# Kernel optimization log

Measured on AMD Instinct MI355X. Metric: run time of the kernel, lower is better.

Reference implementation:

```python
import jax, jax.numpy as jnp
import numpy as np

EPS = 1e-5

def _lc(x, w, b, stride, pad):
    # x: [B,H,W]; w: [Ho,Wo,kh,kw]; b: [Ho,Wo]
    Ho, Wo, kh, kw = w.shape
    patches = jax.lax.conv_general_dilated_patches(
        x[:, None], (kh, kw), (stride, stride), [(pad, pad), (pad, pad)])
    # patches: [B, kh*kw, Ho, Wo]
    out = jnp.einsum('bkij,ijk->bij', patches, w.reshape(Ho, Wo, kh * kw))
    return out + b

def _ln2d(x, g, b):
    # torch LayerNorm over the last two (spatial) dims
    mu = x.mean(axis=(1, 2), keepdims=True)
    var = ((x - mu) ** 2).mean(axis=(1, 2), keepdims=True)
    return (x - mu) * jax.lax.rsqrt(var + EPS) * g + b

def _pool(x):
    # MaxPool2d(kernel=2, stride=2) over spatial dims of [B,H,W]
    return jax.lax.reduce_window(x, -jnp.inf, jax.lax.max, (1, 2, 2), (1, 2, 2), 'VALID')

def setup_inputs() -> dict:
    key = jax.random.key(0)
    ks = jax.random.split(key, 32)
    d = {}
    d['x'] = jax.random.normal(ks[0], (64, 128, 128), jnp.float32)
    sizes = [(128, 7), (64, 5), (64, 5), (32, 3), (32, 3), (16, 3)]
    for i, (s, k) in enumerate(sizes, start=1):
        d[f'w{i}'] = jax.random.normal(ks[4 * i], (s, s, k, k), jnp.float32) / k
        d[f'b{i}'] = jax.random.normal(ks[4 * i + 1], (s, s), jnp.float32)
        d[f'g{i}'] = jnp.ones((s, s), jnp.float32)
        d[f'be{i}'] = jnp.zeros((s, s), jnp.float32)
    d['fcw'] = jax.random.normal(ks[30], (1024, 256), jnp.float32) / np.sqrt(256.0)
    d['fcb'] = jax.random.normal(ks[31], (1024,), jnp.float32) * 0.01
    return d

def reference(x, w1, b1, g1, be1, w2, b2, g2, be2, w3, b3, g3, be3,
              w4, b4, g4, be4, w5, b5, g5, be5, w6, b6, g6, be6, fcw, fcb):
    # dropout is identity (eval / p=0)
    h = _pool(_ln2d(jax.nn.relu(_lc(x, w1, b1, 1, 3)), g1, be1))   # [B,64,64]
    h = _ln2d(jax.nn.relu(_lc(h, w2, b2, 1, 2)), g2, be2)          # [B,64,64]
    h = _pool(_ln2d(jax.nn.relu(_lc(h, w3, b3, 1, 2)), g3, be3))   # [B,32,32]
    h = _ln2d(jax.nn.relu(_lc(h, w4, b4, 1, 1)), g4, be4)          # [B,32,32]
    h = _pool(_ln2d(jax.nn.relu(_lc(h, w5, b5, 1, 1)), g5, be5))   # [B,16,16]
    h = _ln2d(jax.nn.relu(_lc(h, w6, b6, 1, 1)), g6, be6)          # [B,16,16]
    h = h.reshape(h.shape[0], -1) @ fcw.T + fcb                    # [B,1024]
    return jax.nn.softmax(h, axis=-1)
```

## Files before the change

kernel.cpp:

```cpp
#include <hip/hip_runtime.h>

#define LN_EPS 1e-5f

template<int RIN, bool POOL, bool FIRST, int K, int TILE, int S>
__launch_bounds__(256)
__global__ void lc_stage(const float* __restrict__ in,
                         const float* __restrict__ pstats,
                         const float* __restrict__ gamma,
                         const float* __restrict__ beta,
                         const float* __restrict__ w,
                         const float* __restrict__ bias,
                         float* __restrict__ out,
                         float* __restrict__ stats)
{
    constexpr int CIN  = POOL ? RIN / 2 : RIN;
    constexpr int ROUT = CIN;
    constexpr int PAD  = (K - 1) / 2;
    constexpr int RT   = TILE + K - 1;
    constexpr int PP   = RT * RT + 1;
    constexpr int NBLK = ROUT / TILE;
    constexpr int WCNT = TILE * TILE * K * K;
    constexpr int SG   = 64 / S;
    constexpr int PG   = 256 / S;
    constexpr int OPT  = (TILE * TILE >= PG) ? (TILE * TILE) / PG : 1;
    constexpr float INV_NPREV = 1.0f / (float)(RIN * RIN);

    struct WB { float w[WCNT]; float b[TILE * TILE]; };
    union UU { WB wb; float red[512]; };

    __shared__ float s_in[S * PP];
    __shared__ UU    s_u;
    __shared__ float s_mean[S], s_rstd[S];

    const int tid = threadIdx.x;
    const int bt  = blockIdx.x % (NBLK * NBLK);
    const int sg  = blockIdx.x / (NBLK * NBLK);
    const int i0  = (bt / NBLK) * TILE;
    const int j0  = (bt % NBLK) * TILE;
    const int S0  = sg * S;

    if constexpr (!FIRST) {
        if (tid < S) {
            float mu  = pstats[S0 + tid] * INV_NPREV;
            float msq = pstats[64 + S0 + tid] * INV_NPREV;
            s_mean[tid] = mu;
            s_rstd[tid] = 1.0f / sqrtf(msq - mu * mu + LN_EPS);
        }
        __syncthreads();
    }

    for (int idx = tid; idx < WCNT; idx += 256) {
        int pi = idx / (K * K);
        int kk = idx % (K * K);
        int gi = i0 + pi / TILE, gj = j0 + pi % TILE;
        s_u.wb.w[idx] = w[(gi * ROUT + gj) * (K * K) + kk];
    }
    if (tid < TILE * TILE) {
        int gi = i0 + tid / TILE, gj = j0 + tid % TILE;
        s_u.wb.b[tid] = bias[gi * ROUT + gj];
    }

    for (int idx = tid; idx < S * RT * RT; idx += 256) {
        int ls = idx / (RT * RT);
        int p  = idx % (RT * RT);
        int rr = p / RT, rc = p % RT;
        int ci = i0 - PAD + rr, cj = j0 - PAD + rc;
        float val = 0.0f;
        if (ci >= 0 && ci < CIN && cj >= 0 && cj < CIN) {
            if constexpr (FIRST) {
                val = in[(S0 + ls) * RIN * RIN + ci * RIN + cj];
            } else if constexpr (POOL) {
                float mu = s_mean[ls], rs = s_rstd[ls];
                float best = -3.4e38f;
                #pragma unroll
                for (int dy = 0; dy < 2; dy++) {
                    #pragma unroll
                    for (int dx = 0; dx < 2; dx++) {
                        int ry = 2 * ci + dy, rx = 2 * cj + dx;
                        float raw = in[(S0 + ls) * RIN * RIN + ry * RIN + rx];
                        float n = (raw - mu) * rs * gamma[ry * RIN + rx] + beta[ry * RIN + rx];
                        best = fmaxf(best, n);
                    }
                }
                val = best;
            } else {
                float mu = s_mean[ls], rs = s_rstd[ls];
                float raw = in[(S0 + ls) * RIN * RIN + ci * RIN + cj];
                val = (raw - mu) * rs * gamma[ci * RIN + cj] + beta[ci * RIN + cj];
            }
        }
        s_in[ls * PP + p] = val;
    }
    __syncthreads();

    const int s  = tid % S;
    const int pg = tid / S;
    const int p0 = pg * OPT;
    float lsum = 0.0f, lsq = 0.0f;
    if (p0 < TILE * TILE) {
        const int ti  = p0 / TILE;
        const int tj0 = p0 % TILE;
        float acc[OPT];
        #pragma unroll
        for (int o = 0; o < OPT; o++) acc[o] = s_u.wb.b[p0 + o];
        #pragma unroll
        for (int ki = 0; ki < K; ki++) {
            float row[OPT + K - 1];
            #pragma unroll
            for (int c = 0; c < OPT + K - 1; c++)
                row[c] = s_in[s * PP + (ti + ki) * RT + tj0 + c];
            #pragma unroll
            for (int kj = 0; kj < K; kj++)
                #pragma unroll
                for (int o = 0; o < OPT; o++)
                    acc[o] += row[o + kj] * s_u.wb.w[(p0 + o) * (K * K) + ki * K + kj];
        }
        #pragma unroll
        for (int o = 0; o < OPT; o++) {
            float v = fmaxf(acc[o], 0.0f);
            out[(S0 + s) * ROUT * ROUT + (i0 + ti) * ROUT + (j0 + tj0 + o)] = v;
            lsum += v;
            lsq  += v * v;
        }
    }

    __syncthreads();
    s_u.red[tid]       = lsum;
    s_u.red[256 + tid] = lsq;
    __syncthreads();
    if (tid < S) {
        float a = 0.0f, b = 0.0f;
        #pragma unroll
        for (int g = 0; g < PG; g++) {
            a += s_u.red[g * S + tid];
            b += s_u.red[256 + g * S + tid];
        }
        atomicAdd(&stats[S0 + tid], a);
        atomicAdd(&stats[64 + S0 + tid], b);
    }
}

__launch_bounds__(256)
__global__ void fc_logits(const float* __restrict__ t6,
                          const float* __restrict__ stats6,
                          const float* __restrict__ g6,
                          const float* __restrict__ be6,
                          const float* __restrict__ fcw,
                          const float* __restrict__ fcb,
                          float* __restrict__ logits)
{
    __shared__ float h[256];
    const int s   = blockIdx.x >> 2;
    const int q   = blockIdx.x & 3;
    const int tid = threadIdx.x;

    float mu  = stats6[s] * (1.0f / 256.0f);
    float msq = stats6[64 + s] * (1.0f / 256.0f);
    float rstd = 1.0f / sqrtf(msq - mu * mu + LN_EPS);
    h[tid] = (t6[s * 256 + tid] - mu) * rstd * g6[tid] + be6[tid];
    __syncthreads();

    const int o = q * 256 + tid;
    const float4* wr = (const float4*)(fcw + o * 256);
    float acc = 0.0f;
    #pragma unroll 8
    for (int k = 0; k < 64; k++) {
        float4 wv = wr[k];
        acc += wv.x * h[4 * k] + wv.y * h[4 * k + 1] + wv.z * h[4 * k + 2] + wv.w * h[4 * k + 3];
    }
    logits[s * 1024 + o] = acc + fcb[o];
}

__launch_bounds__(256)
__global__ void softmax_k(const float* __restrict__ logits,
                          float* __restrict__ out)
{
    __shared__ float red[256];
    const int s   = blockIdx.x;
    const int tid = threadIdx.x;

    float4 v = ((const float4*)(logits + s * 1024))[tid];
    float lmax = fmaxf(fmaxf(v.x, v.y), fmaxf(v.z, v.w));
    red[tid] = lmax;
    __syncthreads();
    for (int off = 128; off > 0; off >>= 1) {
        if (tid < off) red[tid] = fmaxf(red[tid], red[tid + off]);
        __syncthreads();
    }
    float M = red[0];
    __syncthreads();

    float4 e;
    e.x = expf(v.x - M); e.y = expf(v.y - M);
    e.z = expf(v.z - M); e.w = expf(v.w - M);
    red[tid] = e.x + e.y + e.z + e.w;
    __syncthreads();
    for (int off = 128; off > 0; off >>= 1) {
        if (tid < off) red[tid] += red[tid + off];
        __syncthreads();
    }
    float inv = 1.0f / red[0];
    e.x *= inv; e.y *= inv; e.z *= inv; e.w *= inv;
    ((float4*)(out + s * 1024))[tid] = e;
}

extern "C" void kernel_launch(void* const* d_in, const int* in_sizes, int n_in,
                              void* d_out, int out_size, void* d_ws, size_t ws_size,
                              hipStream_t stream) {
    (void)in_sizes; (void)n_in; (void)out_size; (void)ws_size;

    const float* x   = (const float*)d_in[0];
    const float* w1  = (const float*)d_in[1];
    const float* b1  = (const float*)d_in[2];
    const float* g1  = (const float*)d_in[3];
    const float* be1 = (const float*)d_in[4];
    const float* w2  = (const float*)d_in[5];
    const float* b2  = (const float*)d_in[6];
    const float* g2  = (const float*)d_in[7];
    const float* be2 = (const float*)d_in[8];
    const float* w3  = (const float*)d_in[9];
    const float* b3  = (const float*)d_in[10];
    const float* g3  = (const float*)d_in[11];
    const float* be3 = (const float*)d_in[12];
    const float* w4  = (const float*)d_in[13];
    const float* b4  = (const float*)d_in[14];
    const float* g4  = (const float*)d_in[15];
    const float* be4 = (const float*)d_in[16];
    const float* w5  = (const float*)d_in[17];
    const float* b5  = (const float*)d_in[18];
    const float* g5  = (const float*)d_in[19];
    const float* be5 = (const float*)d_in[20];
    const float* w6  = (const float*)d_in[21];
    const float* b6  = (const float*)d_in[22];
    const float* g6  = (const float*)d_in[23];
    const float* be6 = (const float*)d_in[24];
    const float* fcw = (const float*)d_in[25];
    const float* fcb = (const float*)d_in[26];

    float* ws = (float*)d_ws;
    float* t1 = ws;
    float* t2 = t1 + 64 * 128 * 128;
    float* t3 = t2 + 64 * 64 * 64;
    float* t4 = t3 + 64 * 64 * 64;
    float* t5 = t4 + 64 * 32 * 32;
    float* t6 = t5 + 64 * 32 * 32;
    float* st = t6 + 64 * 16 * 16;

    hipMemsetAsync(st, 0, 6 * 128 * sizeof(float), stream);

    lc_stage<128, false, true,  7, 8, 16><<<1024, 256, 0, stream>>>(x,  nullptr,  nullptr, nullptr, w1, b1, t1, st + 0);
    lc_stage<128, true,  false, 5, 4, 16><<<1024, 256, 0, stream>>>(t1, st + 0,   g1, be1, w2, b2, t2, st + 128);
    lc_stage<64,  false, false, 5, 4, 16><<<1024, 256, 0, stream>>>(t2, st + 128, g2, be2, w3, b3, t3, st + 256);
    lc_stage<64,  true,  false, 3, 4, 16><<<256,  256, 0, stream>>>(t3, st + 256, g3, be3, w4, b4, t4, st + 384);
    lc_stage<32,  false, false, 3, 4, 16><<<256,  256, 0, stream>>>(t4, st + 384, g4, be4, w5, b5, t5, st + 512);
    lc_stage<32,  true,  false, 3, 4, 4><<<256,   256, 0, stream>>>(t5, st + 512, g5, be5, w6, b6, t6, st + 640);
    fc_logits<<<256, 256, 0, stream>>>(t6, st + 640, g6, be6, fcw, fcb, t1);
    softmax_k<<<64, 256, 0, stream>>>(t1, (float*)d_out);
}
```

Baseline: 184.3 us.

## Fuse all stages into one persistent cooperative kernel with grid syncs

Replaces the eight separate kernel launches with a single cooperative persistent kernel of 512 blocks that loops over work units and uses grid-wide syncs between layers. Per-stage tile and sample-group sizes are retuned so that stage 1 uses 32 samples per block and stages 2-3 use 8x8 tiles. The FC stage now processes four samples per block so each weight row is read once per group of samples. This removes launch gaps and repeated weight loads, at the cost of grid-sync overhead and occupancy limits from the large static shared buffer.

```diff
diff --git a/kernel.cpp b/kernel.cpp
--- a/kernel.cpp
+++ b/kernel.cpp
@@ -1,207 +1,263 @@
 #include <hip/hip_runtime.h>
+#include <hip/hip_cooperative_groups.h>
+
+namespace cg = cooperative_groups;
 
 #define LN_EPS 1e-5f
 
+constexpr int GRID_BLOCKS = 512;
+constexpr int SMEM_FLOATS = 10368;
+
+struct Params {
+    const float* x;
+    const float *w1,*b1,*g1,*be1;
+    const float *w2,*b2,*g2,*be2;
+    const float *w3,*b3,*g3,*be3;
+    const float *w4,*b4,*g4,*be4;
+    const float *w5,*b5,*g5,*be5;
+    const float *w6,*b6,*g6,*be6;
+    const float *fcw,*fcb;
+    float* out;
+    float* ws;
+};
+
 template<int RIN, bool POOL, bool FIRST, int K, int TILE, int S>
-__launch_bounds__(256)
-__global__ void lc_stage(const float* __restrict__ in,
-                         const float* __restrict__ pstats,
-                         const float* __restrict__ gamma,
-                         const float* __restrict__ beta,
-                         const float* __restrict__ w,
-                         const float* __restrict__ bias,
-                         float* __restrict__ out,
-                         float* __restrict__ stats)
-{
-    constexpr int CIN  = POOL ? RIN / 2 : RIN;
+__device__ void lc_stage_dev(float* sm,
+                             const float* __restrict__ in,
+                             const float* __restrict__ pstats,
+                             const float* __restrict__ gamma,
+                             const float* __restrict__ beta,
+                             const float* __restrict__ w,
+                             const float* __restrict__ bias,
+                             float* __restrict__ out,
+                             float* __restrict__ stats)
+{
+    constexpr int CIN  = POOL ? RIN/2 : RIN;
     constexpr int ROUT = CIN;
-    constexpr int PAD  = (K - 1) / 2;
+    constexpr int PAD  = (K-1)/2;
     constexpr int RT   = TILE + K - 1;
-    constexpr int PP   = RT * RT + 1;
+    constexpr int PP   = RT*RT + 1;
     constexpr int NBLK = ROUT / TILE;
-    constexpr int WCNT = TILE * TILE * K * K;
+    constexpr int WCNT = TILE*TILE*K*K;
     constexpr int SG   = 64 / S;
     constexpr int PG   = 256 / S;
-    constexpr int OPT  = (TILE * TILE >= PG) ? (TILE * TILE) / PG : 1;
-    constexpr float INV_NPREV = 1.0f / (float)(RIN * RIN);
-
-    struct WB { float w[WCNT]; float b[TILE * TILE]; };
-    union UU { WB wb; float red[512]; };
-
-    __shared__ float s_in[S * PP];
-    __shared__ UU    s_u;
-    __shared__ float s_mean[S], s_rstd[S];
+    constexpr int OPT  = (TILE*TILE) / PG;
+    constexpr int NUNIT= NBLK*NBLK*SG;
+    constexpr float INV_NPREV = 1.0f / (float)(RIN*RIN);
+    static_assert(PG*OPT == TILE*TILE, "position mapping must cover tile");
+
+    float* s_in = sm;
+    float* s_w  = sm + S*PP;
+    float* s_b  = s_w + WCNT;
+    float* s_mr = s_b + TILE*TILE;
+    float* s_red= s_mr + 2*S;
 
     const int tid = threadIdx.x;
-    const int bt  = blockIdx.x % (NBLK * NBLK);
-    const int sg  = blockIdx.x / (NBLK * NBLK);
-    const int i0  = (bt / NBLK) * TILE;
-    const int j0  = (bt % NBLK) * TILE;
-    const int S0  = sg * S;
-
-    if constexpr (!FIRST) {
-        if (tid < S) {
-            float mu  = pstats[S0 + tid] * INV_NPREV;
-            float msq = pstats[64 + S0 + tid] * INV_NPREV;
-            s_mean[tid] = mu;
-            s_rstd[tid] = 1.0f / sqrtf(msq - mu * mu + LN_EPS);
-        }
-        __syncthreads();
-    }
-
-    for (int idx = tid; idx < WCNT; idx += 256) {
-        int pi = idx / (K * K);
-        int kk = idx % (K * K);
-        int gi = i0 + pi / TILE, gj = j0 + pi % TILE;
-        s_u.wb.w[idx] = w[(gi * ROUT + gj) * (K * K) + kk];
-    }
-    if (tid < TILE * TILE) {
-        int gi = i0 + tid / TILE, gj = j0 + tid % TILE;
-        s_u.wb.b[tid] = bias[gi * ROUT + gj];
-    }
-
-    for (int idx = tid; idx < S * RT * RT; idx += 256) {
-        int ls = idx / (RT * RT);
-        int p  = idx % (RT * RT);
-        int rr = p / RT, rc = p % RT;
-        int ci = i0 - PAD + rr, cj = j0 - PAD + rc;
-        float val = 0.0f;
-        if (ci >= 0 && ci < CIN && cj >= 0 && cj < CIN) {
-            if constexpr (FIRST) {
-                val = in[(S0 + ls) * RIN * RIN + ci * RIN + cj];
-            } else if constexpr (POOL) {
-                float mu = s_mean[ls], rs = s_rstd[ls];
-                float best = -3.4e38f;
-                #pragma unroll
-                for (int dy = 0; dy < 2; dy++) {
+
+    for (int unit = blockIdx.x; unit < NUNIT; unit += gridDim.x) {
+        const int bt = unit % (NBLK*NBLK);
+        const int sg = unit / (NBLK*NBLK);
+        const int i0 = (bt / NBLK) * TILE;
+        const int j0 = (bt % NBLK) * TILE;
+        const int S0 = sg * S;
+
+        if constexpr (!FIRST) {
+            if (tid < S) {
+                float mu  = pstats[S0 + tid] * INV_NPREV;
+                float msq = pstats[64 + S0 + tid] * INV_NPREV;
+                s_mr[tid]     = mu;
+                s_mr[S + tid] = rsqrtf(msq - mu*mu + LN_EPS);
+            }
+        }
+        for (int idx = tid; idx < WCNT; idx += 256) {
+            int pi = idx / (K*K);
+            int kk = idx % (K*K);
+            int gi = i0 + pi / TILE, gj = j0 + pi % TILE;
+            s_w[idx] = w[(gi*ROUT + gj)*(K*K) + kk];
+        }
+        if (tid < TILE*TILE) {
+            int gi = i0 + tid / TILE, gj = j0 + tid % TILE;
+            s_b[tid] = bias[gi*ROUT + gj];
+        }
+        __syncthreads();
+
+        for (int idx = tid; idx < S*RT*RT; idx += 256) {
+            int ls = idx / (RT*RT);
+            int p  = idx % (RT*RT);
+            int rr = p / RT, rc = p % RT;
+            int ci = i0 - PAD + rr, cj = j0 - PAD + rc;
+            float val = 0.0f;
+            if (ci >= 0 && ci < CIN && cj >= 0 && cj < CIN) {
+                if constexpr (FIRST) {
+                    val = in[(S0+ls)*RIN*RIN + ci*RIN + cj];
+                } else if constexpr (POOL) {
+                    float mu = s_mr[ls], rs = s_mr[S+ls];
+                    float best = -3.4e38f;
+                    #pragma unroll
+                    for (int dy = 0; dy < 2; dy++)
                     #pragma unroll
                     for (int dx = 0; dx < 2; dx++) {
-                        int ry = 2 * ci + dy, rx = 2 * cj + dx;
-                        float raw = in[(S0 + ls) * RIN * RIN + ry * RIN + rx];
-                        float n = (raw - mu) * rs * gamma[ry * RIN + rx] + beta[ry * RIN + rx];
+                        int ry = 2*ci+dy, rx = 2*cj+dx;
+                        float raw = in[(S0+ls)*RIN*RIN + ry*RIN + rx];
+                        float n = (raw-mu)*rs*gamma[ry*RIN+rx] + beta[ry*RIN+rx];
                         best = fmaxf(best, n);
                     }
+                    val = best;
+                } else {
+                    float mu = s_mr[ls], rs = s_mr[S+ls];
+                    float raw = in[(S0+ls)*RIN*RIN + ci*RIN + cj];
+                    val = (raw-mu)*rs*gamma[ci*RIN+cj] + beta[ci*RIN+cj];
                 }
-                val = best;
-            } else {
-                float mu = s_mean[ls], rs = s_rstd[ls];
-                float raw = in[(S0 + ls) * RIN * RIN + ci * RIN + cj];
-                val = (raw - mu) * rs * gamma[ci * RIN + cj] + beta[ci * RIN + cj];
-            }
-        }
-        s_in[ls * PP + p] = val;
-    }
-    __syncthreads();
-
-    const int s  = tid % S;
-    const int pg = tid / S;
-    const int p0 = pg * OPT;
-    float lsum = 0.0f, lsq = 0.0f;
-    if (p0 < TILE * TILE) {
+            }
+            s_in[ls*PP + p] = val;
+        }
+        __syncthreads();
+
+        const int s   = tid % S;
+        const int pg  = tid / S;
+        const int p0  = pg * OPT;
         const int ti  = p0 / TILE;
         const int tj0 = p0 % TILE;
-        float acc[OPT];
+        float lsum = 0.f, lsq = 0.f;
+        {
+            float acc[OPT];
+            #pragma unroll
+            for (int o = 0; o < OPT; o++) acc[o] = s_b[p0+o];
+            #pragma unroll
+            for (int ki = 0; ki < K; ki++) {
+                float row[OPT+K-1];
+                #pragma unroll
+                for (int c = 0; c < OPT+K-1; c++)
+                    row[c] = s_in[s*PP + (ti+ki)*RT + tj0 + c];
+                #pragma unroll
+                for (int kj = 0; kj < K; kj++)
+                    #pragma unroll
+                    for (int o = 0; o < OPT; o++)
+                        acc[o] += row[o+kj] * s_w[(p0+o)*(K*K) + ki*K + kj];
+            }
+            #pragma unroll
+            for (int o = 0; o < OPT; o++) {
+                float v = fmaxf(acc[o], 0.f);
+                out[(S0+s)*ROUT*ROUT + (i0+ti)*ROUT + (j0+tj0+o)] = v;
+                lsum += v; lsq += v*v;
+            }
+        }
+
+        s_red[tid]     = lsum;
+        s_red[256+tid] = lsq;
+        __syncthreads();
+        if (tid < S) {
+            float a = 0.f, b = 0.f;
+            #pragma unroll
+            for (int g = 0; g < PG; g++) { a += s_red[g*S+tid]; b += s_red[256+g*S+tid]; }
+            atomicAdd(&stats[S0+tid], a);
+            atomicAdd(&stats[64+S0+tid], b);
+        }
+        __syncthreads();
+    }
+}
+
+__device__ void fc_dev(float* sm, const float* __restrict__ t6,
+                       const float* __restrict__ stats6,
+                       const float* __restrict__ g6, const float* __restrict__ be6,
+                       const float* __restrict__ fcw, const float* __restrict__ fcb,
+                       float* __restrict__ logits)
+{
+    float* h = sm;
+    const int tid = threadIdx.x;
+    for (int unit = blockIdx.x; unit < 64; unit += gridDim.x) {
+        const int sg = unit >> 2;
+        const int q  = unit & 3;
         #pragma unroll
-        for (int o = 0; o < OPT; o++) acc[o] = s_u.wb.b[p0 + o];
-        #pragma unroll
-        for (int ki = 0; ki < K; ki++) {
-            float row[OPT + K - 1];
-            #pragma unroll
-            for (int c = 0; c < OPT + K - 1; c++)
-                row[c] = s_in[s * PP + (ti + ki) * RT + tj0 + c];
-            #pragma unroll
-            for (int kj = 0; kj < K; kj++)
-                #pragma unroll
-                for (int o = 0; o < OPT; o++)
-                    acc[o] += row[o + kj] * s_u.wb.w[(p0 + o) * (K * K) + ki * K + kj];
-        }
-        #pragma unroll
-        for (int o = 0; o < OPT; o++) {
-            float v = fmaxf(acc[o], 0.0f);
-            out[(S0 + s) * ROUT * ROUT + (i0 + ti) * ROUT + (j0 + tj0 + o)] = v;
-            lsum += v;
-            lsq  += v * v;
-        }
+        for (int r = 0; r < 4; r++) {
+            int smp = sg*4 + r;
+            float mu  = stats6[smp] * (1.f/256.f);
+            float msq = stats6[64+smp] * (1.f/256.f);
+            float rstd = rsqrtf(msq - mu*mu + LN_EPS);
+            h[r*256 + tid] = (t6[smp*256 + tid] - mu)*rstd*g6[tid] + be6[tid];
+        }
+        __syncthreads();
+        const int o = q*256 + tid;
+        const float4* wr = (const float4*)(fcw + o*256);
+        const float4* h4 = (const float4*)h;
+        float a0=0.f, a1=0.f, a2=0.f, a3=0.f;
+        #pragma unroll 4
+        for (int k = 0; k < 64; k++) {
+            float4 wv = wr[k];
+            float4 h0 = h4[k], h1 = h4[64+k], h2 = h4[128+k], h3 = h4[192+k];
+            a0 += wv.x*h0.x + wv.y*h0.y + wv.z*h0.z + wv.w*h0.w;
+            a1 += wv.x*h1.x + wv.y*h1.y + wv.z*h1.z + wv.w*h1.w;
+            a2 += wv.x*h2.x + wv.y*h2.y + wv.z*h2.z + wv.w*h2.w;
+            a3 += wv.x*h3.x + wv.y*h3.y + wv.z*h3.z + wv.w*h3.w;
+        }
+        float bo = fcb[o];
+        logits[(sg*4+0)*1024 + o] = a0 + bo;
+        logits[(sg*4+1)*1024 + o] = a1 + bo;
+        logits[(sg*4+2)*1024 + o] = a2 + bo;
+        logits[(sg*4+3)*1024 + o] = a3 + bo;
+        __syncthreads();
     }
-
-    __syncthreads();
-    s_u.red[tid]       = lsum;
-    s_u.red[256 + tid] = lsq;
-    __syncthreads();
-    if (tid < S) {
-        float a = 0.0f, b = 0.0f;
-        #pragma unroll
-        for (int g = 0; g < PG; g++) {
-            a += s_u.red[g * S + tid];
-            b += s_u.red[256 + g * S + tid];
-        }
-        atomicAdd(&stats[S0 + tid], a);
-        atomicAdd(&stats[64 + S0 + tid], b);
+}
+
+__device__ void softmax_dev(float* sm, const float* __restrict__ logits,
+                            float* __restrict__ outp)
+{
+    float* red = sm;
+    const int tid = threadIdx.x;
+    for (int unit = blockIdx.x; unit < 64; unit += gridDim.x) {
+        float4 v = ((const float4*)(logits + unit*1024))[tid];
+        float lmax = fmaxf(fmaxf(v.x,v.y), fmaxf(v.z,v.w));
+        red[tid] = lmax;
+        __syncthreads();
+        for (int off=128; off>0; off>>=1) {
+            if (tid<off) red[tid]=fmaxf(red[tid],red[tid+off]);
+            __syncthreads();
+        }
+        float M = red[0];
+        __syncthreads();
+        float4 e;
+        e.x=expf(v.x-M); e.y=expf(v.y-M); e.z=expf(v.z-M); e.w=expf(v.w-M);
+        red[tid] = e.x+e.y+e.z+e.w;
+        __syncthreads();
+        for (int off=128; off>0; off>>=1) {
+            if (tid<off) red[tid]+=red[tid+off];
+            __syncthreads();
+        }
+        float inv = 1.0f/red[0];
+        e.x*=inv; e.y*=inv; e.z*=inv; e.w*=inv;
+        ((float4*)(outp + unit*1024))[tid] = e;
+        __syncthreads();
     }
 }
 
-__launch_bounds__(256)
-__global__ void fc_logits(const float* __restrict__ t6,
-                          const float* __restrict__ stats6,
-                          const float* __restrict__ g6,
-                          const float* __restrict__ be6,
-                          const float* __restrict__ fcw,
-                          const float* __restrict__ fcb,
-                          float* __restrict__ logits)
-{
-    __shared__ float h[256];
-    const int s   = blockIdx.x >> 2;
-    const int q   = blockIdx.x & 3;
-    const int tid = threadIdx.x;
-
-    float mu  = stats6[s] * (1.0f / 256.0f);
-    float msq = stats6[64 + s] * (1.0f / 256.0f);
-    float rstd = 1.0f / sqrtf(msq - mu * mu + LN_EPS);
-    h[tid] = (t6[s * 256 + tid] - mu) * rstd * g6[tid] + be6[tid];
-    __syncthreads();
-
-    const int o = q * 256 + tid;
-    const float4* wr = (const float4*)(fcw + o * 256);
-    float acc = 0.0f;
-    #pragma unroll 8
-    for (int k = 0; k < 64; k++) {
-        float4 wv = wr[k];
-        acc += wv.x * h[4 * k] + wv.y * h[4 * k + 1] + wv.z * h[4 * k + 2] + wv.w * h[4 * k + 3];
-    }
-    logits[s * 1024 + o] = acc + fcb[o];
-}
-
-__launch_bounds__(256)
-__global__ void softmax_k(const float* __restrict__ logits,
-                          float* __restrict__ out)
-{
-    __shared__ float red[256];
-    const int s   = blockIdx.x;
-    const int tid = threadIdx.x;
-
-    float4 v = ((const float4*)(logits + s * 1024))[tid];
-    float lmax = fmaxf(fmaxf(v.x, v.y), fmaxf(v.z, v.w));
-    red[tid] = lmax;
-    __syncthreads();
-    for (int off = 128; off > 0; off >>= 1) {
-        if (tid < off) red[tid] = fmaxf(red[tid], red[tid + off]);
-        __syncthreads();
-    }
-    float M = red[0];
-    __syncthreads();
-
-    float4 e;
-    e.x = expf(v.x - M); e.y = expf(v.y - M);
-    e.z = expf(v.z - M); e.w = expf(v.w - M);
-    red[tid] = e.x + e.y + e.z + e.w;
-    __syncthreads();
-    for (int off = 128; off > 0; off >>= 1) {
-        if (tid < off) red[tid] += red[tid + off];
-        __syncthreads();
-    }
-    float inv = 1.0f / red[0];
-    e.x *= inv; e.y *= inv; e.z *= inv; e.w *= inv;
-    ((float4*)(out + s * 1024))[tid] = e;
+__global__ __launch_bounds__(256, 2) void allnet(Params p)
+{
+    __shared__ __align__(16) float sm[SMEM_FLOATS];
+    cg::grid_group grid = cg::this_grid();
+
+    float* t1 = p.ws;
+    float* t2 = t1 + 64*128*128;
+    float* t3 = t2 + 64*64*64;
+    float* t4 = t3 + 64*64*64;
+    float* t5 = t4 + 64*32*32;
+    float* t6 = t5 + 64*32*32;
+    float* st = t6 + 64*16*16;
+
+    lc_stage_dev<128,false,true, 7,8,32>(sm, p.x, nullptr, nullptr, nullptr, p.w1, p.b1, t1, st);
+    grid.sync();
+    lc_stage_dev<128,true, false,5,8,8 >(sm, t1, st,     p.g1, p.be1, p.w2, p.b2, t2, st+128);
+    grid.sync();
+    lc_stage_dev<64, false,false,5,8,8 >(sm, t2, st+128, p.g2, p.be2, p.w3, p.b3, t3, st+256);
+    grid.sync();
+    lc_stage_dev<64, true, false,3,4,16>(sm, t3, st+256, p.g3, p.be3, p.w4, p.b4, t4, st+384);
+    grid.sync();
+    lc_stage_dev<32, false,false,3,4,16>(sm, t4, st+384, p.g4, p.be4, p.w5, p.b5, t5, st+512);
+    grid.sync();
+    lc_stage_dev<32, true, false,3,4,16>(sm, t5, st+512, p.g5, p.be5, p.w6, p.b6, t6, st+640);
+    grid.sync();
+    fc_dev(sm, t6, st+640, p.g6, p.be6, p.fcw, p.fcb, t1);
+    grid.sync();
+    softmax_dev(sm, t1, p.out);
 }
 
 extern "C" void kernel_launch(void* const* d_in, const int* in_sizes, int n_in,
@@ -209,51 +265,28 @@
                               hipStream_t stream) {
     (void)in_sizes; (void)n_in; (void)out_size; (void)ws_size;
 
-    const float* x   = (const float*)d_in[0];
-    const float* w1  = (const float*)d_in[1];
-    const float* b1  = (const float*)d_in[2];
-    const float* g1  = (const float*)d_in[3];
-    const float* be1 = (const float*)d_in[4];
-    const float* w2  = (const float*)d_in[5];
-    const float* b2  = (const float*)d_in[6];
-    const float* g2  = (const float*)d_in[7];
-    const float* be2 = (const float*)d_in[8];
-    const float* w3  = (const float*)d_in[9];
-    const float* b3  = (const float*)d_in[10];
-    const float* g3  = (const float*)d_in[11];
-    const float* be3 = (const float*)d_in[12];
-    const float* w4  = (const float*)d_in[13];
-    const float* b4  = (const float*)d_in[14];
-    const float* g4  = (const float*)d_in[15];
-    const float* be4 = (const float*)d_in[16];
-    const float* w5  = (const float*)d_in[17];
-    const float* b5  = (const float*)d_in[18];
-    const float* g5  = (const float*)d_in[19];
-    const float* be5 = (const float*)d_in[20];
-    const float* w6  = (const float*)d_in[21];
-    const float* b6  = (const float*)d_in[22];
-    const float* g6  = (const float*)d_in[23];
-    const float* be6 = (const float*)d_in[24];
-    const float* fcw = (const float*)d_in[25];
-    const float* fcb = (const float*)d_in[26];
-
-    float* ws = (float*)d_ws;
-    float* t1 = ws;
-    float* t2 = t1 + 64 * 128 * 128;
-    float* t3 = t2 + 64 * 64 * 64;
-    float* t4 = t3 + 64 * 64 * 64;
-    float* t5 = t4 + 64 * 32 * 32;
-    float* t6 = t5 + 64 * 32 * 32;
-    float* st = t6 + 64 * 16 * 16;
-
+    Params p;
+    p.x   = (const float*)d_in[0];
+    p.w1  = (const float*)d_in[1];  p.b1  = (const float*)d_in[2];
+    p.g1  = (const float*)d_in[3];  p.be1 = (const float*)d_in[4];
+    p.w2  = (const float*)d_in[5];  p.b2  = (const float*)d_in[6];
+    p.g2  = (const float*)d_in[7];  p.be2 = (const float*)d_in[8];
+    p.w3  = (const float*)d_in[9];  p.b3  = (const float*)d_in[10];
+    p.g3  = (const float*)d_in[11]; p.be3 = (const float*)d_in[12];
+    p.w4  = (const float*)d_in[13]; p.b4  = (const float*)d_in[14];
+    p.g4  = (const float*)d_in[15]; p.be4 = (const float*)d_in[16];
+    p.w5  = (const float*)d_in[17]; p.b5  = (const float*)d_in[18];
+    p.g5  = (const float*)d_in[19]; p.be5 = (const float*)d_in[20];
+    p.w6  = (const float*)d_in[21]; p.b6  = (const float*)d_in[22];
+    p.g6  = (const float*)d_in[23]; p.be6 = (const float*)d_in[24];
+    p.fcw = (const float*)d_in[25]; p.fcb = (const float*)d_in[26];
+    p.out = (float*)d_out;
+    p.ws  = (float*)d_ws;
+
+    float* st = p.ws + 64*128*128 + 2*(64*64*64) + 2*(64*32*32) + 64*16*16;
     hipMemsetAsync(st, 0, 6 * 128 * sizeof(float), stream);
 
-    lc_stage<128, false, true,  7, 8, 16><<<1024, 256, 0, stream>>>(x,  nullptr,  nullptr, nullptr, w1, b1, t1, st + 0);
-    lc_stage<128, true,  false, 5, 4, 16><<<1024, 256, 0, stream>>>(t1, st + 0,   g1, be1, w2, b2, t2, st + 128);
-    lc_stage<64,  false, false, 5, 4, 16><<<1024, 256, 0, stream>>>(t2, st + 128, g2, be2, w3, b3, t3, st + 256);
-    lc_stage<64,  true,  false, 3, 4, 16><<<256,  256, 0, stream>>>(t3, st + 256, g3, be3, w4, b4, t4, st + 384);
-    lc_stage<32,  false, false, 3, 4, 16><<<256,  256, 0, stream>>>(t4, st + 384, g4, be4, w5, b5, t5, st + 512);
-    lc_stage<32,  true,  false, 3, 4, 4><<<256,   256, 0, stream>>>(t5, st + 512, g5, be5, w6, b6, t6, st + 640);
-    fc_logits<<<256, 256, 0, stream>>>(t6, st + 640, g6, be6, fcw, fcb, t1);
-    softmax_k<<<64, 256, 0, stream>>>(t1, (float*)d_out);
-}
+    void* args[] = { (void*)&p };
+    hipLaunchCooperativeKernel((void*)allnet, dim3(GRID_BLOCKS), dim3(256),
+                               args, 0, stream);
+}
```

After: 592.6 us. 222% more time.

## Fuse stages two through six, FC and softmax into one per-sample kernel

Applied to the files above, without the earlier changes.

Keeps the first locally connected conv as its own tiled kernel. Everything after it (LayerNorm, pool, the remaining five locally connected layers, the FC layer and softmax) now runs in a single kernel with one block per sample, holding activations in shared memory. LayerNorm statistics are reduced inside the block with wave shuffles instead of global atomics, which also drops the memset. This removes six launches and the global round-trips of intermediate activations, but the tail runs on only 64 blocks and every block reads all weights straight from global memory, so parallelism drops.

```diff
diff --git a/kernel.cpp b/kernel.cpp
--- a/kernel.cpp
+++ b/kernel.cpp
@@ -2,206 +2,297 @@
 
 #define LN_EPS 1e-5f
 
-template<int RIN, bool POOL, bool FIRST, int K, int TILE, int S>
-__launch_bounds__(256)
-__global__ void lc_stage(const float* __restrict__ in,
-                         const float* __restrict__ pstats,
-                         const float* __restrict__ gamma,
-                         const float* __restrict__ beta,
-                         const float* __restrict__ w,
-                         const float* __restrict__ bias,
-                         float* __restrict__ out,
-                         float* __restrict__ stats)
-{
-    constexpr int CIN  = POOL ? RIN / 2 : RIN;
-    constexpr int ROUT = CIN;
-    constexpr int PAD  = (K - 1) / 2;
-    constexpr int RT   = TILE + K - 1;
-    constexpr int PP   = RT * RT + 1;
-    constexpr int NBLK = ROUT / TILE;
+__global__ __launch_bounds__(256) void s1_conv(const float* __restrict__ x,
+                                               const float* __restrict__ w,
+                                               const float* __restrict__ bias,
+                                               float* __restrict__ out)
+{
+    constexpr int R = 128, K = 7, TILE = 8, S = 16, PAD = 3;
+    constexpr int RT = TILE + K - 1;
+    constexpr int PP = RT * RT + 1;
+    constexpr int NBLK = R / TILE;
     constexpr int WCNT = TILE * TILE * K * K;
-    constexpr int SG   = 64 / S;
-    constexpr int PG   = 256 / S;
-    constexpr int OPT  = (TILE * TILE >= PG) ? (TILE * TILE) / PG : 1;
-    constexpr float INV_NPREV = 1.0f / (float)(RIN * RIN);
-
-    struct WB { float w[WCNT]; float b[TILE * TILE]; };
-    union UU { WB wb; float red[512]; };
+    constexpr int PG = 256 / S;
+    constexpr int OPT = TILE * TILE / PG;
 
     __shared__ float s_in[S * PP];
-    __shared__ UU    s_u;
-    __shared__ float s_mean[S], s_rstd[S];
-
-    const int tid = threadIdx.x;
-    const int bt  = blockIdx.x % (NBLK * NBLK);
-    const int sg  = blockIdx.x / (NBLK * NBLK);
-    const int i0  = (bt / NBLK) * TILE;
-    const int j0  = (bt % NBLK) * TILE;
-    const int S0  = sg * S;
-
-    if constexpr (!FIRST) {
-        if (tid < S) {
-            float mu  = pstats[S0 + tid] * INV_NPREV;
-            float msq = pstats[64 + S0 + tid] * INV_NPREV;
-            s_mean[tid] = mu;
-            s_rstd[tid] = 1.0f / sqrtf(msq - mu * mu + LN_EPS);
-        }
-        __syncthreads();
-    }
+    __shared__ float s_w[WCNT];
+    __shared__ float s_b[TILE * TILE];
+
+    const int tid = threadIdx.x;
+    const int bt = blockIdx.x % (NBLK * NBLK);
+    const int sg = blockIdx.x / (NBLK * NBLK);
+    const int i0 = (bt / NBLK) * TILE;
+    const int j0 = (bt % NBLK) * TILE;
+    const int S0 = sg * S;
 
     for (int idx = tid; idx < WCNT; idx += 256) {
-        int pi = idx / (K * K);
-        int kk = idx % (K * K);
+        int pi = idx / (K * K), kk = idx % (K * K);
         int gi = i0 + pi / TILE, gj = j0 + pi % TILE;
-        s_u.wb.w[idx] = w[(gi * ROUT + gj) * (K * K) + kk];
-    }
-    if (tid < TILE * TILE) {
-        int gi = i0 + tid / TILE, gj = j0 + tid % TILE;
-        s_u.wb.b[tid] = bias[gi * ROUT + gj];
-    }
+        s_w[idx] = w[(gi * R + gj) * (K * K) + kk];
+    }
+    if (tid < TILE * TILE)
+        s_b[tid] = bias[(i0 + tid / TILE) * R + (j0 + tid % TILE)];
 
     for (int idx = tid; idx < S * RT * RT; idx += 256) {
-        int ls = idx / (RT * RT);
-        int p  = idx % (RT * RT);
-        int rr = p / RT, rc = p % RT;
-        int ci = i0 - PAD + rr, cj = j0 - PAD + rc;
-        float val = 0.0f;
-        if (ci >= 0 && ci < CIN && cj >= 0 && cj < CIN) {
-            if constexpr (FIRST) {
-                val = in[(S0 + ls) * RIN * RIN + ci * RIN + cj];
-            } else if constexpr (POOL) {
-                float mu = s_mean[ls], rs = s_rstd[ls];
-                float best = -3.4e38f;
-                #pragma unroll
-                for (int dy = 0; dy < 2; dy++) {
-                    #pragma unroll
-                    for (int dx = 0; dx < 2; dx++) {
-                        int ry = 2 * ci + dy, rx = 2 * cj + dx;
-                        float raw = in[(S0 + ls) * RIN * RIN + ry * RIN + rx];
-                        float n = (raw - mu) * rs * gamma[ry * RIN + rx] + beta[ry * RIN + rx];
-                        best = fmaxf(best, n);
-                    }
-                }
-                val = best;
-            } else {
-                float mu = s_mean[ls], rs = s_rstd[ls];
-                float raw = in[(S0 + ls) * RIN * RIN + ci * RIN + cj];
-                val = (raw - mu) * rs * gamma[ci * RIN + cj] + beta[ci * RIN + cj];
-            }
-        }
-        s_in[ls * PP + p] = val;
-    }
-    __syncthreads();
-
-    const int s  = tid % S;
+        int ls = idx / (RT * RT), p = idx % (RT * RT);
+        int ci = i0 - PAD + p / RT, cj = j0 - PAD + p % RT;
+        float v = 0.0f;
+        if (ci >= 0 && ci < R && cj >= 0 && cj < R)
+            v = x[(S0 + ls) * R * R + ci * R + cj];
+        s_in[ls * PP + p] = v;
+    }
+    __syncthreads();
+
+    const int s = tid % S;
     const int pg = tid / S;
     const int p0 = pg * OPT;
-    float lsum = 0.0f, lsq = 0.0f;
-    if (p0 < TILE * TILE) {
-        const int ti  = p0 / TILE;
-        const int tj0 = p0 % TILE;
-        float acc[OPT];
+    const int ti = p0 / TILE, tj0 = p0 % TILE;
+    float acc[OPT];
+    #pragma unroll
+    for (int o = 0; o < OPT; o++) acc[o] = s_b[p0 + o];
+    #pragma unroll
+    for (int ki = 0; ki < K; ki++) {
+        float row[OPT + K - 1];
         #pragma unroll
-        for (int o = 0; o < OPT; o++) acc[o] = s_u.wb.b[p0 + o];
+        for (int c = 0; c < OPT + K - 1; c++)
+            row[c] = s_in[s * PP + (ti + ki) * RT + tj0 + c];
         #pragma unroll
-        for (int ki = 0; ki < K; ki++) {
-            float row[OPT + K - 1];
-            #pragma unroll
-            for (int c = 0; c < OPT + K - 1; c++)
-                row[c] = s_in[s * PP + (ti + ki) * RT + tj0 + c];
-            #pragma unroll
-            for (int kj = 0; kj < K; kj++)
-                #pragma unroll
-                for (int o = 0; o < OPT; o++)
-                    acc[o] += row[o + kj] * s_u.wb.w[(p0 + o) * (K * K) + ki * K + kj];
+        for (int kj = 0; kj < K; kj++)
+            #pragma unroll
+            for (int o = 0; o < OPT; o++)
+                acc[o] += row[o + kj] * s_w[(p0 + o) * (K * K) + ki * K + kj];
+    }
+    #pragma unroll
+    for (int o = 0; o < OPT; o++)
+        out[(S0 + s) * R * R + (i0 + ti) * R + (j0 + tj0 + o)] = fmaxf(acc[o], 0.0f);
+}
+
+__device__ __forceinline__ void stats_reduce(float* red, float lsum, float lsq,
+                                             float inv_n, float* s_mu, float* s_rs)
+{
+    const int tid = threadIdx.x;
+    #pragma unroll
+    for (int off = 32; off > 0; off >>= 1) {
+        lsum += __shfl_down(lsum, off, 64);
+        lsq  += __shfl_down(lsq,  off, 64);
+    }
+    if ((tid & 63) == 0) { red[tid >> 6] = lsum; red[8 + (tid >> 6)] = lsq; }
+    __syncthreads();
+    if (tid == 0) {
+        float a = red[0] + red[1] + red[2] + red[3];
+        float b = red[8] + red[9] + red[10] + red[11];
+        float mu = a * inv_n, ms = b * inv_n;
+        *s_mu = mu;
+        *s_rs = rsqrtf(ms - mu * mu + LN_EPS);
+    }
+    __syncthreads();
+}
+
+template<int M, int K>
+__device__ __forceinline__ void conv_lds(const float* __restrict__ I,
+                                         const float* __restrict__ w,
+                                         const float* __restrict__ bias,
+                                         float* __restrict__ R,
+                                         float& lsum, float& lsq)
+{
+    constexpr int OPT = (M * M) / 256;
+    constexpr int PADK = (K - 1) / 2;
+    constexpr int STR = M + 1;
+    const int tid = threadIdx.x;
+    const int p0 = tid * OPT;
+    const int i = p0 / M, j0 = p0 % M;
+    const float* wb = w + p0 * K * K;
+
+    float acc[OPT];
+    #pragma unroll
+    for (int o = 0; o < OPT; o++) acc[o] = bias[p0 + o];
+    #pragma unroll
+    for (int ki = 0; ki < K; ki++) {
+        int ii = i - PADK + ki;
+        float row[OPT + K - 1];
+        if (ii >= 0 && ii < M) {
+            #pragma unroll
+            for (int c = 0; c < OPT + K - 1; c++) {
+                int jj = j0 - PADK + c;
+                row[c] = (jj >= 0 && jj < M) ? I[ii * STR + jj] : 0.0f;
+            }
+        } else {
+            #pragma unroll
+            for (int c = 0; c < OPT + K - 1; c++) row[c] = 0.0f;
         }
         #pragma unroll
-        for (int o = 0; o < OPT; o++) {
-            float v = fmaxf(acc[o], 0.0f);
-            out[(S0 + s) * ROUT * ROUT + (i0 + ti) * ROUT + (j0 + tj0 + o)] = v;
-            lsum += v;
-            lsq  += v * v;
+        for (int kj = 0; kj < K; kj++)
+            #pragma unroll
+            for (int o = 0; o < OPT; o++)
+                acc[o] += row[o + kj] * wb[o * K * K + ki * K + kj];
+    }
+    #pragma unroll
+    for (int o = 0; o < OPT; o++) {
+        float v = fmaxf(acc[o], 0.0f);
+        R[i * STR + j0 + o] = v;
+        lsum += v;
+        lsq  += v * v;
+    }
+}
+
+template<int N, bool POOL>
+__device__ __forceinline__ void transform(const float* __restrict__ R,
+                                          float mu, float rs,
+                                          const float* __restrict__ g,
+                                          const float* __restrict__ b,
+                                          float* __restrict__ I)
+{
+    constexpr int M = POOL ? N / 2 : N;
+    constexpr int SR = N + 1, SI = M + 1;
+    const int tid = threadIdx.x;
+    for (int p = tid; p < M * M; p += 256) {
+        int i = p / M, j = p % M;
+        float v;
+        if constexpr (POOL) {
+            float best = -3.4e38f;
+            #pragma unroll
+            for (int dy = 0; dy < 2; dy++)
+                #pragma unroll
+                for (int dx = 0; dx < 2; dx++) {
+                    int r = 2 * i + dy, c = 2 * j + dx;
+                    float n = (R[r * SR + c] - mu) * rs * g[r * N + c] + b[r * N + c];
+                    best = fmaxf(best, n);
+                }
+            v = best;
+        } else {
+            v = (R[i * SR + j] - mu) * rs * g[i * N + j] + b[i * N + j];
         }
-    }
-
-    __syncthreads();
-    s_u.red[tid]       = lsum;
-    s_u.red[256 + tid] = lsq;
-    __syncthreads();
-    if (tid < S) {
-        float a = 0.0f, b = 0.0f;
-        #pragma unroll
-        for (int g = 0; g < PG; g++) {
-            a += s_u.red[g * S + tid];
-            b += s_u.red[256 + g * S + tid];
+        I[i * SI + j] = v;
+    }
+}
+
+__global__ __launch_bounds__(256) void tail_fused(
+    const float* __restrict__ t1,
+    const float* __restrict__ g1, const float* __restrict__ be1,
+    const float* __restrict__ w2, const float* __restrict__ b2,
+    const float* __restrict__ g2, const float* __restrict__ be2,
+    const float* __restrict__ w3, const float* __restrict__ b3,
+    const float* __restrict__ g3, const float* __restrict__ be3,
+    const float* __restrict__ w4, const float* __restrict__ b4,
+    const float* __restrict__ g4, const float* __restrict__ be4,
+    const float* __restrict__ w5, const float* __restrict__ b5,
+    const float* __restrict__ g5, const float* __restrict__ be5,
+    const float* __restrict__ w6, const float* __restrict__ b6,
+    const float* __restrict__ g6, const float* __restrict__ be6,
+    const float* __restrict__ fcw, const float* __restrict__ fcb,
+    float* __restrict__ outp)
+{
+    __shared__ __align__(16) float I[64 * 65];
+    __shared__ __align__(16) float R[64 * 65];
+    __shared__ __align__(16) float h[256];
+    __shared__ float red[16];
+    __shared__ float s_mu, s_rs;
+
+    const int s = blockIdx.x;
+    const int tid = threadIdx.x;
+    const float* x1 = t1 + s * 16384;
+
+    float ls = 0.f, lq = 0.f;
+    const float4* x4 = (const float4*)x1;
+    for (int i = tid; i < 4096; i += 256) {
+        float4 v = x4[i];
+        ls += v.x + v.y + v.z + v.w;
+        lq += v.x * v.x + v.y * v.y + v.z * v.z + v.w * v.w;
+    }
+    stats_reduce(red, ls, lq, 1.f / 16384.f, &s_mu, &s_rs);
+
+    {
+        float mu = s_mu, rs = s_rs;
+        for (int p = tid; p < 4096; p += 256) {
+            int i = p >> 6, j = p & 63;
+            float best = -3.4e38f;
+            #pragma unroll
+            for (int dy = 0; dy < 2; dy++)
+                #pragma unroll
+                for (int dx = 0; dx < 2; dx++) {
+                    int r = 2 * i + dy, c = 2 * j + dx;
+                    float n = (x1[r * 128 + c] - mu) * rs * g1[r * 128 + c] + be1[r * 128 + c];
+                    best = fmaxf(best, n);
+                }
+            I[i * 65 + j] = best;
         }
-        atomicAdd(&stats[S0 + tid], a);
-        atomicAdd(&stats[64 + S0 + tid], b);
-    }
-}
-
-__launch_bounds__(256)
-__global__ void fc_logits(const float* __restrict__ t6,
-                          const float* __restrict__ stats6,
-                          const float* __restrict__ g6,
-                          const float* __restrict__ be6,
-                          const float* __restrict__ fcw,
-                          const float* __restrict__ fcb,
-                          float* __restrict__ logits)
-{
-    __shared__ float h[256];
-    const int s   = blockIdx.x >> 2;
-    const int q   = blockIdx.x & 3;
-    const int tid = threadIdx.x;
-
-    float mu  = stats6[s] * (1.0f / 256.0f);
-    float msq = stats6[64 + s] * (1.0f / 256.0f);
-    float rstd = 1.0f / sqrtf(msq - mu * mu + LN_EPS);
-    h[tid] = (t6[s * 256 + tid] - mu) * rstd * g6[tid] + be6[tid];
-    __syncthreads();
-
-    const int o = q * 256 + tid;
-    const float4* wr = (const float4*)(fcw + o * 256);
-    float acc = 0.0f;
-    #pragma unroll 8
-    for (int k = 0; k < 64; k++) {
-        float4 wv = wr[k];
-        acc += wv.x * h[4 * k] + wv.y * h[4 * k + 1] + wv.z * h[4 * k + 2] + wv.w * h[4 * k + 3];
-    }
-    logits[s * 1024 + o] = acc + fcb[o];
-}
-
-__launch_bounds__(256)
-__global__ void softmax_k(const float* __restrict__ logits,
-                          float* __restrict__ out)
-{
-    __shared__ float red[256];
-    const int s   = blockIdx.x;
-    const int tid = threadIdx.x;
-
-    float4 v = ((const float4*)(logits + s * 1024))[tid];
-    float lmax = fmaxf(fmaxf(v.x, v.y), fmaxf(v.z, v.w));
-    red[tid] = lmax;
-    __syncthreads();
-    for (int off = 128; off > 0; off >>= 1) {
-        if (tid < off) red[tid] = fmaxf(red[tid], red[tid + off]);
-        __syncthreads();
-    }
-    float M = red[0];
-    __syncthreads();
-
-    float4 e;
-    e.x = expf(v.x - M); e.y = expf(v.y - M);
-    e.z = expf(v.z - M); e.w = expf(v.w - M);
-    red[tid] = e.x + e.y + e.z + e.w;
-    __syncthreads();
-    for (int off = 128; off > 0; off >>= 1) {
-        if (tid < off) red[tid] += red[tid + off];
-        __syncthreads();
-    }
-    float inv = 1.0f / red[0];
-    e.x *= inv; e.y *= inv; e.z *= inv; e.w *= inv;
-    ((float4*)(out + s * 1024))[tid] = e;
+    }
+    __syncthreads();
+
+    ls = lq = 0.f; conv_lds<64, 5>(I, w2, b2, R, ls, lq);
+    stats_reduce(red, ls, lq, 1.f / 4096.f, &s_mu, &s_rs);
+    transform<64, false>(R, s_mu, s_rs, g2, be2, I);
+    __syncthreads();
+
+    ls = lq = 0.f; conv_lds<64, 5>(I, w3, b3, R, ls, lq);
+    stats_reduce(red, ls, lq, 1.f / 4096.f, &s_mu, &s_rs);
+    transform<64, true>(R, s_mu, s_rs, g3, be3, I);
+    __syncthreads();
+
+    ls = lq = 0.f; conv_lds<32, 3>(I, w4, b4, R, ls, lq);
+    stats_reduce(red, ls, lq, 1.f / 1024.f, &s_mu, &s_rs);
+    transform<32, false>(R, s_mu, s_rs, g4, be4, I);
+    __syncthreads();
+
+    ls = lq = 0.f; conv_lds<32, 3>(I, w5, b5, R, ls, lq);
+    stats_reduce(red, ls, lq, 1.f / 1024.f, &s_mu, &s_rs);
+    transform<32, true>(R, s_mu, s_rs, g5, be5, I);
+    __syncthreads();
+
+    ls = lq = 0.f; conv_lds<16, 3>(I, w6, b6, R, ls, lq);
+    stats_reduce(red, ls, lq, 1.f / 256.f, &s_mu, &s_rs);
+
+    {
+        int i = tid >> 4, j = tid & 15;
+        h[tid] = (R[i * 17 + j] - s_mu) * s_rs * g6[tid] + be6[tid];
+    }
+    __syncthreads();
+
+    const float4* h4 = (const float4*)h;
+    float la[4];
+    float lmax = -3.4e38f;
+    #pragma unroll
+    for (int r = 0; r < 4; r++) {
+        int o = r * 256 + tid;
+        const float4* wr = (const float4*)(fcw + o * 256);
+        float acc = 0.f;
+        #pragma unroll 8
+        for (int k = 0; k < 64; k++) {
+            float4 wv = wr[k];
+            float4 hv = h4[k];
+            acc += wv.x * hv.x + wv.y * hv.y + wv.z * hv.z + wv.w * hv.w;
+        }
+        acc += fcb[o];
+        la[r] = acc;
+        lmax = fmaxf(lmax, acc);
+    }
+    #pragma unroll
+    for (int off = 32; off > 0; off >>= 1)
+        lmax = fmaxf(lmax, __shfl_down(lmax, off, 64));
+    if ((tid & 63) == 0) red[tid >> 6] = lmax;
+    __syncthreads();
+    if (tid == 0)
+        s_mu = fmaxf(fmaxf(red[0], red[1]), fmaxf(red[2], red[3]));
+    __syncthreads();
+    float M = s_mu;
+
+    float e[4];
+    float lsum = 0.f;
+    #pragma unroll
+    for (int r = 0; r < 4; r++) { e[r] = expf(la[r] - M); lsum += e[r]; }
+    #pragma unroll
+    for (int off = 32; off > 0; off >>= 1)
+        lsum += __shfl_down(lsum, off, 64);
+    if ((tid & 63) == 0) red[8 + (tid >> 6)] = lsum;
+    __syncthreads();
+    if (tid == 0)
+        s_rs = 1.0f / (red[8] + red[9] + red[10] + red[11]);
+    __syncthreads();
+    float inv = s_rs;
+    #pragma unroll
+    for (int r = 0; r < 4; r++)
+        outp[s * 1024 + r * 256 + tid] = e[r] * inv;
 }
 
 extern "C" void kernel_launch(void* const* d_in, const int* in_sizes, int n_in,
@@ -210,50 +301,25 @@
     (void)in_sizes; (void)n_in; (void)out_size; (void)ws_size;
 
     const float* x   = (const float*)d_in[0];
-    const float* w1  = (const float*)d_in[1];
-    const float* b1  = (const float*)d_in[2];
-    const float* g1  = (const float*)d_in[3];
-    const float* be1 = (const float*)d_in[4];
-    const float* w2  = (const float*)d_in[5];
-    const float* b2  = (const float*)d_in[6];
-    const float* g2  = (const float*)d_in[7];
-    const float* be2 = (const float*)d_in[8];
-    const float* w3  = (const float*)d_in[9];
-    const float* b3  = (const float*)d_in[10];
-    const float* g3  = (const float*)d_in[11];
-    const float* be3 = (const float*)d_in[12];
-    const float* w4  = (const float*)d_in[13];
-    const float* b4  = (const float*)d_in[14];
-    const float* g4  = (const float*)d_in[15];
-    const float* be4 = (const float*)d_in[16];
-    const float* w5  = (const float*)d_in[17];
-    const float* b5  = (const float*)d_in[18];
-    const float* g5  = (const float*)d_in[19];
-    const float* be5 = (const float*)d_in[20];
-    const float* w6  = (const float*)d_in[21];
-    const float* b6  = (const float*)d_in[22];
-    const float* g6  = (const float*)d_in[23];
-    const float* be6 = (const float*)d_in[24];
-    const float* fcw = (const float*)d_in[25];
-    const float* fcb = (const float*)d_in[26];
-
-    float* ws = (float*)d_ws;
-    float* t1 = ws;
-    float* t2 = t1 + 64 * 128 * 128;
-    float* t3 = t2 + 64 * 64 * 64;
-    float* t4 = t3 + 64 * 64 * 64;
-    float* t5 = t4 + 64 * 32 * 32;
-    float* t6 = t5 + 64 * 32 * 32;
-    float* st = t6 + 64 * 16 * 16;
-
-    hipMemsetAsync(st, 0, 6 * 128 * sizeof(float), stream);
-
-    lc_stage<128, false, true,  7, 8, 16><<<1024, 256, 0, stream>>>(x,  nullptr,  nullptr, nullptr, w1, b1, t1, st + 0);
-    lc_stage<128, true,  false, 5, 4, 16><<<1024, 256, 0, stream>>>(t1, st + 0,   g1, be1, w2, b2, t2, st + 128);
-    lc_stage<64,  false, false, 5, 4, 16><<<1024, 256, 0, stream>>>(t2, st + 128, g2, be2, w3, b3, t3, st + 256);
-    lc_stage<64,  true,  false, 3, 4, 16><<<256,  256, 0, stream>>>(t3, st + 256, g3, be3, w4, b4, t4, st + 384);
-    lc_stage<32,  false, false, 3, 4, 16><<<256,  256, 0, stream>>>(t4, st + 384, g4, be4, w5, b5, t5, st + 512);
-    lc_stage<32,  true,  false, 3, 4, 4><<<256,   256, 0, stream>>>(t5, st + 512, g5, be5, w6, b6, t6, st + 640);
-    fc_logits<<<256, 256, 0, stream>>>(t6, st + 640, g6, be6, fcw, fcb, t1);
-    softmax_k<<<64, 256, 0, stream>>>(t1, (float*)d_out);
-}
+    const float* w1  = (const float*)d_in[1];  const float* b1  = (const float*)d_in[2];
+    const float* g1  = (const float*)d_in[3];  const float* be1 = (const float*)d_in[4];
+    const float* w2  = (const float*)d_in[5];  const float* b2  = (const float*)d_in[6];
+    const float* g2  = (const float*)d_in[7];  const float* be2 = (const float*)d_in[8];
+    const float* w3  = (const float*)d_in[9];  const float* b3  = (const float*)d_in[10];
+    const float* g3  = (const float*)d_in[11]; const float* be3 = (const float*)d_in[12];
+    const float* w4  = (const float*)d_in[13]; const float* b4  = (const float*)d_in[14];
+    const float* g4  = (const float*)d_in[15]; const float* be4 = (const float*)d_in[16];
+    const float* w5  = (const float*)d_in[17]; const float* b5  = (const float*)d_in[18];
+    const float* g5  = (const float*)d_in[19]; const float* be5 = (const float*)d_in[20];
+    const float* w6  = (const float*)d_in[21]; const float* b6  = (const float*)d_in[22];
+    const float* g6  = (const float*)d_in[23]; const float* be6 = (const float*)d_in[24];
+    const float* fcw = (const float*)d_in[25]; const float* fcb = (const float*)d_in[26];
+
+    float* t1 = (float*)d_ws;
+
+    s1_conv<<<1024, 256, 0, stream>>>(x, w1, b1, t1);
+    tail_fused<<<64, 256, 0, stream>>>(t1,
+        g1, be1, w2, b2, g2, be2, w3, b3, g3, be3,
+        w4, b4, g4, be4, w5, b5, g5, be5, w6, b6, g6, be6,
+        fcw, fcb, (float*)d_out);
+}
```

Measured after the change: 200.1 us. +8.6%, slower.
